# Optimization experiments

Measured on AMD Instinct MI355X. Metric: run time of the kernel, lower is better.

## Reference

```python
import jax, jax.numpy as jnp
import numpy as np

N, E, IN_CH, HIDDEN, N_CLASS, LAYERS = 2048, 1024, 512, 512, 40, 10
EPS = 1e-10


def setup_inputs() -> dict:
    key = jax.random.key(0)
    ks = jax.random.split(key, 6)
    x = jax.random.normal(ks[0], (1, N, IN_CH), jnp.float32)
    H = (jax.random.uniform(ks[1], (N, E)) < 0.02).astype(jnp.float32)
    # symmetric Laplacian-like operator so eigh is meaningful
    M = jax.random.normal(ks[2], (1, N, N), jnp.float32) / np.sqrt(N).astype(np.float32)
    L = 0.5 * (M + jnp.swapaxes(M, 1, 2))
    W_first = jax.random.normal(ks[3], (HIDDEN, IN_CH), jnp.float32) * 0.05
    W_mid = jax.random.normal(ks[4], (LAYERS - 2, HIDDEN, HIDDEN), jnp.float32) * 0.05
    W_last = jax.random.normal(ks[5], (N_CLASS, HIDDEN), jnp.float32) * 0.05
    return {"x": x, "L": L, "H": H, "W_first": W_first, "W_mid": W_mid, "W_last": W_last}


def _expanded_energy(x2d, H, d_v, d_e):
    # Vectorized form of the nested hyperedge/pair loop:
    # sum_e sum_{u<v in e} H_ue*H_ve/(d_e+eps) * ||x_u/sqrt(dv_u+eps) - x_v/sqrt(dv_v+eps)||^2
    # = sum_e (s_e * q_e - ||m_e||^2) / (d_e + eps)  with binary H (w_e = 1)
    y = x2d / jnp.sqrt(d_v + EPS)[:, None]          # [N, F]
    q = H.T @ jnp.sum(y * y, axis=1)                # [E] sum_u H_ue ||y_u||^2
    m = H.T @ y                                     # [E, F]
    s = jnp.sum(H, axis=0)                          # [E] edge degrees (= d_e)
    return jnp.sum((s * q - jnp.sum(m * m, axis=1)) / (d_e + EPS))


def reference(x, L, H, W_first, W_mid, W_last):
    weights = [W_first] + [W_mid[i] for i in range(LAYERS - 2)] + [W_last]
    d_v = jnp.sum(H, axis=1)
    d_e = jnp.sum(H, axis=0)
    # eigh of L is identical every layer in the original; compute once
    eigvals = jnp.linalg.eigh(L)[0]                 # [B, N]
    spectral_gap = jnp.min(jnp.where(eigvals > 1e-10, eigvals, jnp.inf))
    energies, energies_exp, snorms = [], [], []
    for i, W in enumerate(weights):
        x = jax.nn.relu(jnp.einsum('bnm,bmf->bnf', L, x) @ W.T)
        xs, Ls = x[0], L[0]                         # @torch.no_grad() blocks
        energies.append(jnp.trace(xs.T @ (Ls @ xs)))
        energies_exp.append(_expanded_energy(xs, H, d_v, d_e))
        snorms.append(jnp.linalg.norm(W, ord=2))
        # dropout skipped (eval-mode reference)
    log_probs = jax.nn.log_softmax(x, axis=1)       # dim=1 as in original
    return (log_probs, jnp.stack(energies), jnp.stack(energies_exp),
            jnp.stack(snorms), spectral_gap)
```

## Files before the change

### kernel.cpp

```cpp
#include <hip/hip_runtime.h>
#include <math.h>


typedef __attribute__((ext_vector_type(8))) short short8;
typedef __attribute__((ext_vector_type(4))) float f32x4;

#define NSHIFT 256

__device__ inline ushort bf16_rne(float f) {
    unsigned int u = __float_as_uint(f);
    return (ushort)((u + 0x7FFFu + ((u >> 16) & 1u)) >> 16);
}
__device__ inline float bf16_tof(ushort h) {
    return __uint_as_float(((unsigned int)h) << 16);
}

__device__ __forceinline__ void pbar(int* bar, int e, int w, int nwg) {
    __syncthreads();
    if (threadIdx.x == 0) {
        __threadfence();
        __hip_atomic_store(bar + 16 + w*16, e, __ATOMIC_RELAXED, __HIP_MEMORY_SCOPE_AGENT);
    }
    if (w == 0) {
        if ((int)threadIdx.x < nwg) {
            while (__hip_atomic_load(bar + 16 + threadIdx.x*16, __ATOMIC_RELAXED,
                                     __HIP_MEMORY_SCOPE_AGENT) < e)
                __builtin_amdgcn_s_sleep(1);
        }
        __syncthreads();
        if (threadIdx.x == 0)
            __hip_atomic_store(bar, e, __ATOMIC_RELEASE, __HIP_MEMORY_SCOPE_AGENT);
    } else {
        if (threadIdx.x == 0) {
            while (__hip_atomic_load(bar, __ATOMIC_RELAXED, __HIP_MEMORY_SCOPE_AGENT) < e)
                __builtin_amdgcn_s_sleep(8);
        }
    }
    if (threadIdx.x == 0) __threadfence();
    __syncthreads();
}

__global__ void init_misc(int* bar) {
    for (int j = blockIdx.x*256 + threadIdx.x; j < 16384; j += gridDim.x*256) bar[j] = 0;
}

template<bool TA, bool TB>
__device__ __forceinline__
void tile64g(const float* __restrict__ A, int lda,
             const float* __restrict__ B, int ldb,
             int bm, int bn, int k0, int k1, float acc[4][4],
             float (*sA)[68], float (*sB)[68])
{
    const int tid = threadIdx.x;
    const int tx = tid & 15, ty = tid >> 4;
    for (int kk = k0; kk < k1; kk += 16) {
        __syncthreads();
        for (int i = tid; i < 1024; i += 256) {
            int m, k2;
            if (TA) { m = i & 63; k2 = i >> 6; } else { k2 = i & 15; m = i >> 4; }
            sA[k2][m] = TA ? A[(size_t)(kk + k2)*lda + bm + m]
                           : A[(size_t)(bm + m)*lda + kk + k2];
        }
        for (int i = tid; i < 1024; i += 256) {
            int n, k2;
            if (TB) { k2 = i & 15; n = i >> 4; } else { n = i & 63; k2 = i >> 6; }
            sB[k2][n] = TB ? B[(size_t)(bn + n)*ldb + kk + k2]
                           : B[(size_t)(kk + k2)*ldb + bn + n];
        }
        __syncthreads();
        #pragma unroll
        for (int k2 = 0; k2 < 16; ++k2) {
            float4 a4 = *(const float4*)&sA[k2][ty*4];
            float4 b4 = *(const float4*)&sB[k2][tx*4];
            float av[4] = {a4.x, a4.y, a4.z, a4.w};
            float bv[4] = {b4.x, b4.y, b4.z, b4.w};
            #pragma unroll
            for (int i2 = 0; i2 < 4; ++i2)
                #pragma unroll
                for (int j2 = 0; j2 < 4; ++j2)
                    acc[i2][j2] += av[i2] * bv[j2];
        }
    }
}

template<bool TA, bool TB>
__device__ __forceinline__
void tile64d(const float* __restrict__ A, int lda,
             const float* __restrict__ B, int ldb,
             int bm, int bn, int k0, int k1, float acc[4][4],
             float (*sA)[16][68], float (*sB)[16][68])
{
    const int tid = threadIdx.x;
    const int tx = tid & 15, ty = tid >> 4;
    float ra[4], rb[4];
    auto ldregs = [&](int kk) {
        #pragma unroll
        for (int q = 0; q < 4; ++q) {
            int i = tid + q*256;
            if (TA) { int m = i & 63, k2 = i >> 6; ra[q] = A[(size_t)(kk + k2)*lda + bm + m]; }
            else    { int k2 = i & 15, m = i >> 4; ra[q] = A[(size_t)(bm + m)*lda + kk + k2]; }
            if (TB) { int k3 = i & 15, n = i >> 4; rb[q] = B[(size_t)(bn + n)*ldb + kk + k3]; }
            else    { int k3 = i >> 6, n = i & 63; rb[q] = B[(size_t)(kk + k3)*ldb + bn + n]; }
        }
    };
    auto stlds = [&](int buf) {
        #pragma unroll
        for (int q = 0; q < 4; ++q) {
            int i = tid + q*256;
            if (TA) { int m = i & 63, k2 = i >> 6; sA[buf][k2][m] = ra[q]; }
            else    { int k2 = i & 15, m = i >> 4; sA[buf][k2][m] = ra[q]; }
            if (TB) { int k3 = i & 15, n = i >> 4; sB[buf][k3][n] = rb[q]; }
            else    { int k3 = i >> 6, n = i & 63; sB[buf][k3][n] = rb[q]; }
        }
    };
    const int nit = (k1 - k0) >> 4;
    ldregs(k0);
    stlds(0);
    for (int it = 0; it < nit; ++it) {
        const int buf = it & 1;
        if (it + 1 < nit) ldregs(k0 + (it + 1)*16);
        __syncthreads();
        #pragma unroll
        for (int k2 = 0; k2 < 16; ++k2) {
            float4 a4 = *(const float4*)&sA[buf][k2][ty*4];
            float4 b4 = *(const float4*)&sB[buf][k2][tx*4];
            float av[4] = {a4.x, a4.y, a4.z, a4.w};
            float bv[4] = {b4.x, b4.y, b4.z, b4.w};
            #pragma unroll
            for (int i2 = 0; i2 < 4; ++i2)
                #pragma unroll
                for (int j2 = 0; j2 < 4; ++j2)
                    acc[i2][j2] += av[i2] * bv[j2];
        }
        if (it + 1 < nit) { __syncthreads(); stlds(buf ^ 1); }
    }
}

__device__ __forceinline__ void store_tile(float* C, int ldc, int bm, float acc[4][4]) {
    int tx = threadIdx.x & 15, ty = threadIdx.x >> 4;
    #pragma unroll
    for (int i = 0; i < 4; ++i)
        #pragma unroll
        for (int j = 0; j < 4; ++j)
            C[(size_t)(bm + ty*4 + i)*ldc + tx*4 + j] = acc[i][j];
}

__global__ void init_q0(float* Q) {
    int idx = blockIdx.x*256 + threadIdx.x;
    if (idx < 2048*64) {
        int n = idx >> 6, c = idx & 63;
        Q[(size_t)n*2048 + c] = (n == c) ? 1.f : 0.f;
    }
}

__global__ __launch_bounds__(256)
void lz_LQ(const float* __restrict__ Lm, const float* __restrict__ Qs, float* __restrict__ Cp)
{
    __shared__ float sA[2][16][68], sB[2][16][68];
    int z = blockIdx.x, mt = blockIdx.y;
    float acc[4][4] = {};
    tile64d<false,false>(Lm, 2048, Qs, 2048, mt*64, 0, z*256, z*256 + 256, acc, sA, sB);
    store_tile(Cp + (size_t)z*131072, 64, mt*64, acc);
}

__global__ void lz_sumZ(const float* __restrict__ Cp, float* __restrict__ Z)
{
    int idx = blockIdx.x*256 + threadIdx.x;
    float v = 0.f;
    #pragma unroll
    for (int z = 0; z < 8; ++z) v += Cp[(size_t)z*131072 + idx];
    Z[idx] = v;
}

__global__ __launch_bounds__(256)
void lz_QTZ(const float* __restrict__ Qall, const float* __restrict__ Z, float* __restrict__ Cp)
{
    __shared__ float sA[2][16][68], sB[2][16][68];
    int z = blockIdx.x, b = blockIdx.y;
    float acc[4][4] = {};
    tile64d<true,false>(Qall, 2048, Z, 64, b*64, 0, z*256, z*256 + 256, acc, sA, sB);
    store_tile(Cp + (size_t)z*131072, 64, b*64, acc);
}

__global__ void lz_sumC(const float* __restrict__ Cp, float* __restrict__ Creo,
                        float* __restrict__ Ab, int s)
{
    int idx = blockIdx.x*256 + threadIdx.x;
    float v = 0.f;
    #pragma unroll
    for (int z = 0; z < 8; ++z) v += Cp[(size_t)z*131072 + idx];
    Creo[idx] = v;
    if ((idx >> 6) >= 64*s) Ab[(size_t)s*4096 + (idx - s*4096)] = v;
}

__global__ __launch_bounds__(256)
void lz_QC(const float* __restrict__ Qall, const float* __restrict__ Creo,
           float* __restrict__ Cp, int s)
{
    __shared__ float sA[2][16][68], sB[2][16][68];
    int z = blockIdx.x, mt = blockIdx.y;
    float acc[4][4] = {};
    for (int j = z; j <= s; j += 8)
        tile64d<false,false>(Qall, 2048, Creo, 64, mt*64, 0, j*64, j*64 + 64, acc, sA, sB);
    store_tile(Cp + (size_t)z*131072, 64, mt*64, acc);
}

__global__ __launch_bounds__(256)
void lz_finZ(float* __restrict__ Z, const float* __restrict__ Cp, int nz,
             double* __restrict__ Gp)
{
    __shared__ float zb[64][65];
    int w = blockIdx.x, tid = threadIdx.x;
    for (int idx = tid; idx < 4096; idx += 256) {
        size_t o = (size_t)w*4096 + idx;
        float v = Z[o];
        for (int z = 0; z < nz; ++z) v -= Cp[(size_t)z*131072 + o];
        Z[o] = v;
        zb[idx >> 6][idx & 63] = v;
    }
    __syncthreads();
    int tx = tid & 15, ty = tid >> 4;
    double acc[4][4] = {};
    for (int r = 0; r < 64; ++r) {
        float av[4], bv[4];
        #pragma unroll
        for (int q = 0; q < 4; ++q) { av[q] = zb[r][ty*4 + q]; bv[q] = zb[r][tx*4 + q]; }
        #pragma unroll
        for (int i = 0; i < 4; ++i)
            #pragma unroll
            for (int j = 0; j < 4; ++j)
                acc[i][j] += (double)av[i] * (double)bv[j];
    }
    #pragma unroll
    for (int i = 0; i < 4; ++i)
        #pragma unroll
        for (int j = 0; j < 4; ++j)
            Gp[(size_t)w*4096 + (size_t)(ty*4 + i)*64 + tx*4 + j] = acc[i][j];
}

__global__ __launch_bounds__(256)
void lz_chol(const double* __restrict__ Gp, float* __restrict__ RinvF, float* __restrict__ BbS)
{
    __shared__ double G[64][65];
    __shared__ double Xs[64][65];
    __shared__ double lv[64];
    int tid = threadIdx.x;
    for (int idx = tid; idx < 4096; idx += 256) {
        double g = 0.0;
        for (int z = 0; z < 32; ++z) g += Gp[(size_t)z*4096 + idx];
        G[idx>>6][idx&63] = g;
    }
    __syncthreads();
    for (int k = 0; k < 64; ++k) {
        if (tid < 64) {
            double rkk = sqrt(fmax(G[k][k], 1e-40));
            lv[tid] = (tid == k) ? rkk : ((tid > k) ? G[k][tid]/rkk : 0.0);
        }
        __syncthreads();
        if (tid < 64 && tid >= k) G[k][tid] = lv[tid];
        for (int idx = tid; idx < 4096; idx += 256) {
            int i = idx>>6, j = idx&63;
            if (i > k && j >= i) G[i][j] -= lv[i]*lv[j];
        }
        __syncthreads();
    }
    for (int idx = tid; idx < 4096; idx += 256) {
        int i = idx>>6, j = idx&63;
        BbS[idx] = (j >= i) ? (float)G[i][j] : 0.f;
        Xs[i][j] = 0.0;
    }
    __syncthreads();
    if (tid < 64) {
        int j = tid;
        for (int i = j; i >= 0; --i) {
            double s2 = (i == j) ? 1.0 : 0.0;
            for (int k2 = i + 1; k2 <= j; ++k2) s2 -= G[i][k2]*Xs[k2][j];
            Xs[i][j] = s2 / G[i][i];
        }
    }
    __syncthreads();
    for (int idx = tid; idx < 4096; idx += 256)
        RinvF[idx] = (float)Xs[idx>>6][idx&63];
}

__global__ __launch_bounds__(256)
void lz_apply(const float* __restrict__ Z, const float* __restrict__ Rinv, float* __restrict__ Qn)
{
    __shared__ float sA[2][16][68], sB[2][16][68];
    int w = blockIdx.x;
    float acc[4][4] = {};
    tile64d<false,false>(Z, 64, Rinv, 64, w*64, 0, 0, 64, acc, sA, sB);
    store_tile(Qn, 2048, w*64, acc);
}

__global__ void assemble_band(const float* Ab, const float* Bb, float* band) {
    int idx = blockIdx.x*256 + threadIdx.x;
    if (idx >= 2048*65) return;
    int c = idx / 65, r = idx % 65;
    int row = c + r;
    float v = 0.f;
    if (row < 2048) {
        int j = c >> 6, q = c & 63, rr = q + r;
        if (rr <= 63) {
            const float* A = Ab + (size_t)j*4096;
            v = 0.5f*(A[rr*64 + q] + A[q*64 + rr]);
        } else if (j < 31) {
            int p = rr - 64;
            v = Bb[(size_t)j*4096 + p*64 + q];
        }
    }
    band[idx] = v;
}

__device__ __forceinline__
void pack_item(int idx, const float* __restrict__ src, const float* __restrict__ dv,
               ushort* __restrict__ Bh, ushort* __restrict__ Bl,
               ushort* __restrict__ Ch, ushort* __restrict__ Cl)
{
    int l = idx & 63, t = idx >> 6;
    int nb = t & 31, kc = t >> 5;
    int col = nb*16 + (l & 15);
    int k0 = kc*32 + ((l >> 4) << 3);
    ushort h8[8], l8[8], sh8[8], sl8[8];
    #pragma unroll
    for (int j = 0; j < 8; ++j) {
        int k = k0 + j;
        float v = src[(size_t)k*512 + col];
        ushort hb = bf16_rne(v);
        h8[j] = hb; l8[j] = bf16_rne(v - bf16_tof(hb));
        if (Ch) {
            float t2 = v * (1.0f / sqrtf(dv[k] + 1e-10f));
            ushort hb2 = bf16_rne(t2);
            sh8[j] = hb2; sl8[j] = bf16_rne(t2 - bf16_tof(hb2));
        }
    }
    uint4 hv, lv;
    hv.x = (unsigned)h8[0] | ((unsigned)h8[1] << 16);
    hv.y = (unsigned)h8[2] | ((unsigned)h8[3] << 16);
    hv.z = (unsigned)h8[4] | ((unsigned)h8[5] << 16);
    hv.w = (unsigned)h8[6] | ((unsigned)h8[7] << 16);
    lv.x = (unsigned)l8[0] | ((unsigned)l8[1] << 16);
    lv.y = (unsigned)l8[2] | ((unsigned)l8[3] << 16);
    lv.z = (unsigned)l8[4] | ((unsigned)l8[5] << 16);
    lv.w = (unsigned)l8[6] | ((unsigned)l8[7] << 16);
    *(uint4*)(Bh + (size_t)idx*8) = hv;
    *(uint4*)(Bl + (size_t)idx*8) = lv;
    if (Ch) {
        uint4 shv, slv;
        shv.x = (unsigned)sh8[0] | ((unsigned)sh8[1] << 16);
        shv.y = (unsigned)sh8[2] | ((unsigned)sh8[3] << 16);
        shv.z = (unsigned)sh8[4] | ((unsigned)sh8[5] << 16);
        shv.w = (unsigned)sh8[6] | ((unsigned)sh8[7] << 16);
        slv.x = (unsigned)sl8[0] | ((unsigned)sl8[1] << 16);
        slv.y = (unsigned)sl8[2] | ((unsigned)sl8[3] << 16);
        slv.z = (unsigned)sl8[4] | ((unsigned)sl8[5] << 16);
        slv.w = (unsigned)sl8[6] | ((unsigned)sl8[7] << 16);
        *(uint4*)(Ch + (size_t)idx*8) = shv;
        *(uint4*)(Cl + (size_t)idx*8) = slv;
    }
}

__global__ void pack_both(const float* __restrict__ src, const float* __restrict__ dv,
                          ushort* __restrict__ Bh, ushort* __restrict__ Bl,
                          ushort* __restrict__ Ch, ushort* __restrict__ Cl)
{
    int idx = blockIdx.x*256 + threadIdx.x;
    if (idx < 131072) pack_item(idx, src, dv, Bh, Bl, Ch, Cl);
}

__global__ void pack_A_L(const float* __restrict__ src, int Kld, int MB,
                         ushort* __restrict__ Ah, ushort* __restrict__ Al, int total)
{
    int idx = blockIdx.x*256 + threadIdx.x;
    if (idx >= total) return;
    int l = idx & 63, t = idx >> 6;
    int mb = t % MB, kc = t / MB;
    int m = mb*16 + (l & 15);
    int k0 = kc*32 + ((l >> 4) << 3);
    const float* p = src + (size_t)m*Kld + k0;
    float4 a = *(const float4*)p, b = *(const float4*)(p + 4);
    float vv[8] = {a.x,a.y,a.z,a.w,b.x,b.y,b.z,b.w};
    ushort h8[8], l8[8];
    #pragma unroll
    for (int j = 0; j < 8; ++j) {
        ushort hb = bf16_rne(vv[j]);
        h8[j] = hb; l8[j] = bf16_rne(vv[j] - bf16_tof(hb));
    }
    uint4 hv, lv;
    hv.x = (unsigned)h8[0] | ((unsigned)h8[1] << 16);
    hv.y = (unsigned)h8[2] | ((unsigned)h8[3] << 16);
    hv.z = (unsigned)h8[4] | ((unsigned)h8[5] << 16);
    hv.w = (unsigned)h8[6] | ((unsigned)h8[7] << 16);
    lv.x = (unsigned)l8[0] | ((unsigned)l8[1] << 16);
    lv.y = (unsigned)l8[2] | ((unsigned)l8[3] << 16);
    lv.z = (unsigned)l8[4] | ((unsigned)l8[5] << 16);
    lv.w = (unsigned)l8[6] | ((unsigned)l8[7] << 16);
    *(uint4*)(Ah + (size_t)idx*8) = hv;
    *(uint4*)(Al + (size_t)idx*8) = lv;
}

__global__ void pack_A_T(const float* __restrict__ src, int Mld, int MB,
                         ushort* __restrict__ Ah, int total)
{
    int idx = blockIdx.x*256 + threadIdx.x;
    if (idx >= total) return;
    int l = idx & 63, t = idx >> 6;
    int mb = t % MB, kc = t / MB;
    int m = mb*16 + (l & 15);
    int k0 = kc*32 + ((l >> 4) << 3);
    ushort h8[8];
    #pragma unroll
    for (int j = 0; j < 8; ++j)
        h8[j] = bf16_rne(src[(size_t)(k0 + j)*Mld + m]);
    uint4 hv;
    hv.x = (unsigned)h8[0] | ((unsigned)h8[1] << 16);
    hv.y = (unsigned)h8[2] | ((unsigned)h8[3] << 16);
    hv.z = (unsigned)h8[4] | ((unsigned)h8[5] << 16);
    hv.w = (unsigned)h8[6] | ((unsigned)h8[7] << 16);
    *(uint4*)(Ah + (size_t)idx*8) = hv;
}

__device__ __forceinline__
void mfma_task(int t, const ushort* __restrict__ Lph, const ushort* __restrict__ Lpl,
               const ushort* __restrict__ Bh, const ushort* __restrict__ Bl,
               const ushort* __restrict__ Htp,
               const ushort* __restrict__ Bqh, const ushort* __restrict__ Bql,
               float* __restrict__ U, float* __restrict__ ME,
               ushort (*lA)[4096], ushort (*lB)[4096])
{
    const bool isU = (t < 64);
    const ushort* Ah = isU ? Lph : Htp;
    const ushort* Al = isU ? Lpl : nullptr;
    const ushort* Xh = isU ? Bh : Bqh;
    const ushort* Xl = isU ? Bl : Bql;
    float* C = isU ? U : ME;
    const int MB = isU ? 128 : 64;
    const int tmb = (isU ? (t >> 2) : ((t - 64) >> 2)) * 8;
    const int tnb = (t & 3) * 8;
    const int KC = 64;
    const int tid = threadIdx.x;
    const int lane = tid & 63, wave = tid >> 6;
    const int wr = wave >> 1, wc = wave & 1;

    f32x4 acc[4][4];
    #pragma unroll
    for (int i = 0; i < 4; ++i)
        #pragma unroll
        for (int j = 0; j < 4; ++j) acc[i][j] = (f32x4){0.f,0.f,0.f,0.f};

    uint4 rAh[2], rAl[2], rBh[2], rBl[2];
    auto loadregs = [&](int kc) {
        const uint4* pa = (const uint4*)(Ah + ((size_t)kc*MB + tmb)*512);
        rAh[0] = pa[tid]; rAh[1] = pa[tid + 256];
        if (Al) {
            const uint4* pl = (const uint4*)(Al + ((size_t)kc*MB + tmb)*512);
            rAl[0] = pl[tid]; rAl[1] = pl[tid + 256];
        }
        const uint4* pb = (const uint4*)(Xh + ((size_t)kc*32 + tnb)*512);
        rBh[0] = pb[tid]; rBh[1] = pb[tid + 256];
        const uint4* pc = (const uint4*)(Xl + ((size_t)kc*32 + tnb)*512);
        rBl[0] = pc[tid]; rBl[1] = pc[tid + 256];
    };

    loadregs(0);
    for (int kc = 0; kc < KC; ++kc) {
        __syncthreads();
        *(uint4*)&lA[0][tid*8]       = rAh[0];
        *(uint4*)&lA[0][(tid+256)*8] = rAh[1];
        if (Al) {
            *(uint4*)&lA[1][tid*8]       = rAl[0];
            *(uint4*)&lA[1][(tid+256)*8] = rAl[1];
        }
        *(uint4*)&lB[0][tid*8]       = rBh[0];
        *(uint4*)&lB[0][(tid+256)*8] = rBh[1];
        *(uint4*)&lB[1][tid*8]       = rBl[0];
        *(uint4*)&lB[1][(tid+256)*8] = rBl[1];
        if (kc + 1 < KC) loadregs(kc + 1);
        __syncthreads();

        short8 a_h[4], a_l[4], b_h[4], b_l[4];
        #pragma unroll
        for (int i = 0; i < 4; ++i) {
            a_h[i] = *(const short8*)&lA[0][(((wr*4 + i)*64) + lane)*8];
            if (Al) a_l[i] = *(const short8*)&lA[1][(((wr*4 + i)*64) + lane)*8];
        }
        #pragma unroll
        for (int j = 0; j < 4; ++j) {
            b_h[j] = *(const short8*)&lB[0][(((wc*4 + j)*64) + lane)*8];
            b_l[j] = *(const short8*)&lB[1][(((wc*4 + j)*64) + lane)*8];
        }
        #pragma unroll
        for (int i = 0; i < 4; ++i)
            #pragma unroll
            for (int j = 0; j < 4; ++j) {
                acc[i][j] = __builtin_amdgcn_mfma_f32_16x16x32_bf16(a_h[i], b_h[j], acc[i][j], 0, 0, 0);
                acc[i][j] = __builtin_amdgcn_mfma_f32_16x16x32_bf16(a_h[i], b_l[j], acc[i][j], 0, 0, 0);
                if (Al)
                    acc[i][j] = __builtin_amdgcn_mfma_f32_16x16x32_bf16(a_l[i], b_h[j], acc[i][j], 0, 0, 0);
            }
    }
    const int r0 = tmb*16 + wr*64, c0 = tnb*16 + wc*64;
    #pragma unroll
    for (int i = 0; i < 4; ++i)
        #pragma unroll
        for (int j = 0; j < 4; ++j) {
            int row = r0 + i*16 + ((lane >> 4) << 2);
            int col = c0 + j*16 + (lane & 15);
            #pragma unroll
            for (int r = 0; r < 4; ++r)
                C[(size_t)(row + r)*512 + col] = acc[i][j][r];
        }
}

__global__ __launch_bounds__(256, 2)
void mgemm_dual(const ushort* __restrict__ Lph, const ushort* __restrict__ Lpl,
                const ushort* __restrict__ Bh, const ushort* __restrict__ Bl,
                const ushort* __restrict__ Htp,
                const ushort* __restrict__ Bqh, const ushort* __restrict__ Bql,
                float* __restrict__ U, float* __restrict__ ME)
{
    __shared__ ushort lA[2][4096];
    __shared__ ushort lB[2][4096];
    int t = blockIdx.y * 4 + blockIdx.x;
    mfma_task(t, Lph, Lpl, Bh, Bl, Htp, Bqh, Bql, U, ME, lA, lB);
}

__global__ __launch_bounds__(256, 1)
void mlp_persist(float* __restrict__ u, float* __restrict__ h,
                 const float* __restrict__ Wf, const float* __restrict__ Wm,
                 const ushort* __restrict__ Lph, const ushort* __restrict__ Lpl,
                 const ushort* __restrict__ Htp,
                 ushort* __restrict__ bpkh, ushort* __restrict__ bpkl,
                 ushort* __restrict__ bqh, ushort* __restrict__ bql,
                 const float* __restrict__ H, const float* __restrict__ dv,
                 const float* __restrict__ de,
                 float* __restrict__ mEb, float* __restrict__ srow,
                 float* __restrict__ qpart,
                 float* __restrict__ parts512, float* __restrict__ parts16,
                 float* __restrict__ outp, int* __restrict__ bar)
{
    const int w = blockIdx.x, tid = threadIdx.x;
    __shared__ char smem[35072];
    __shared__ float red4[4];
    float (*sA)[68] = (float(*)[68])smem;
    float (*sB)[68] = (float(*)[68])(smem + 4352);
    ushort (*lA)[4096] = (ushort(*)[4096])smem;
    ushort (*lB)[4096] = (ushort(*)[4096])(smem + 16384);
    int ep = 0;

    for (int k = 0; k < 9; ++k) {
        const float* W = (k == 0) ? Wf : Wm + (size_t)(k-1)*262144;
        if (w == 0 && k > 0 && tid < 64) {
            float s = parts512[tid] + parts512[tid+64] + parts512[tid+128] + parts512[tid+192];
            for (int o = 32; o; o >>= 1) s += __shfl_down(s, o, 64);
            float x = (tid < 16) ? parts16[tid] : 0.f;
            for (int o = 32; o; o >>= 1) x += __shfl_down(x, o, 64);
            if (tid == 0) { outp[81920 + k - 1] = s; outp[81930 + k - 1] = x; }
        }
        {
            int mt = w >> 3, nt = w & 7;
            float acc[4][4] = {};
            tile64g<false,true>(u, 512, W, 512, mt*64, nt*64, 0, 512, acc, sA, sB);
            int tx = tid & 15, ty = tid >> 4;
            #pragma unroll
            for (int i = 0; i < 4; ++i)
                #pragma unroll
                for (int j = 0; j < 4; ++j)
                    h[(size_t)(mt*64 + ty*4 + i)*512 + nt*64 + tx*4 + j] = fmaxf(acc[i][j], 0.f);
        }
        pbar(bar, ++ep, w, 256);
        for (int it = w*256 + tid; it < 131072; it += 65536)
            pack_item(it, h, dv, bpkh, bpkl, bqh, bql);
        {
            int lane = tid & 63;
            #pragma unroll
            for (int g = 0; g < 2; ++g) {
                int row = w*8 + g*4 + (tid >> 6);
                float rs = 1.0f / sqrtf(dv[row] + 1e-10f);
                float ss = 0.f;
                for (int f = lane; f < 512; f += 64) {
                    float t2 = h[(size_t)row*512 + f] * rs;
                    ss += t2*t2;
                }
                for (int o = 32; o; o >>= 1) ss += __shfl_down(ss, o, 64);
                if (lane == 0) srow[row] = ss;
            }
        }
        pbar(bar, ++ep, w, 256);
        if (w < 96) {
            mfma_task(w, Lph, Lpl, bpkh, bpkl, Htp, bqh, bql, u, mEb, lA, lB);
        } else if (w < 128) {
            int task = w - 96;
            int e = (task & 3)*256 + tid;
            int zc = task >> 2;
            float s = 0.f;
            for (int n = zc*256; n < zc*256 + 256; ++n) s += H[(size_t)n*1024 + e] * srow[n];
            qpart[(size_t)zc*1024 + e] = s;
        }
        pbar(bar, ++ep, w, 256);
        if (w < 16) {
            int wave = tid >> 6, lane = tid & 63;
            float acc = 0.f;
            for (int t2 = 0; t2 < 16; ++t2) {
                int e = w*64 + wave*16 + t2;
                float me2 = 0.f;
                for (int f = lane; f < 512; f += 64) { float v = mEb[(size_t)e*512 + f]; me2 += v*v; }
                for (int o = 32; o; o >>= 1) me2 += __shfl_down(me2, o, 64);
                if (lane == 0) {
                    float q = 0.f;
                    for (int z = 0; z < 8; ++z) q += qpart[(size_t)z*1024 + e];
                    acc += (de[e]*q - me2) / (de[e] + 1e-10f);
                }
            }
            if (lane == 0) red4[wave] = acc;
            __syncthreads();
            if (tid == 0) parts16[w] = red4[0]+red4[1]+red4[2]+red4[3];
            __syncthreads();
        }
        {
            int lane = tid & 63;
            float dd = 0.f;
            #pragma unroll
            for (int g = 0; g < 2; ++g) {
                int row = w*8 + g*4 + (tid >> 6);
                for (int f = lane; f < 512; f += 64)
                    dd += h[(size_t)row*512 + f] * u[(size_t)row*512 + f];
            }
            for (int o = 32; o; o >>= 1) dd += __shfl_down(dd, o, 64);
            __syncthreads();
            if (lane == 0) red4[tid >> 6] = dd;
            __syncthreads();
            if (tid == 0) parts512[w] = red4[0]+red4[1]+red4[2]+red4[3];
        }
        pbar(bar, ++ep, w, 256);
    }
    if (w == 0 && tid < 64) {
        float s = parts512[tid] + parts512[tid+64] + parts512[tid+128] + parts512[tid+192];
        for (int o = 32; o; o >>= 1) s += __shfl_down(s, o, 64);
        float x = (tid < 16) ? parts16[tid] : 0.f;
        for (int o = 32; o; o >>= 1) x += __shfl_down(x, o, 64);
        if (tid == 0) { outp[81928] = s; outp[81938] = x; }
    }
}

template<bool TA, bool TB>
__global__ __launch_bounds__(256)
void gemm_f32(const float* A, int lda, const float* B, int ldb,
              float* C, int ldc, float* Cpart,
              int M, int N, int K, float alpha, float beta, int relu)
{
    const int S = (int)gridDim.z, z = (int)blockIdx.z;
    const int kchunk = (K + S - 1) / S;
    const int k0 = z * kchunk;
    const int k1 = (K < k0 + kchunk) ? K : (k0 + kchunk);
    const int bm = blockIdx.y * 64, bn = blockIdx.x * 64;
    __shared__ float As[16][68];
    __shared__ float Bs[16][68];
    const int tid = threadIdx.x;
    const int tx = tid & 15, ty = tid >> 4;
    float acc[4][4] = {};
    for (int kk = k0; kk < k1; kk += 16) {
        for (int i = tid; i < 1024; i += 256) {
            int m, k;
            if (TA) { m = i & 63; k = i >> 6; } else { k = i & 15; m = i >> 4; }
            int gm = bm + m, gk = kk + k;
            float v = 0.f;
            if (gm < M && gk < k1) v = TA ? A[(size_t)gk*lda + gm] : A[(size_t)gm*lda + gk];
            As[k][m] = v;
        }
        for (int i = tid; i < 1024; i += 256) {
            int n, k;
            if (TB) { k = i & 15; n = i >> 4; } else { n = i & 63; k = i >> 6; }
            int gn = bn + n, gk = kk + k;
            float v = 0.f;
            if (gn < N && gk < k1) v = TB ? B[(size_t)gn*ldb + gk] : B[(size_t)gk*ldb + gn];
            Bs[k][n] = v;
        }
        __syncthreads();
        #pragma unroll
        for (int k = 0; k < 16; ++k) {
            float4 ra4 = *reinterpret_cast<const float4*>(&As[k][ty*4]);
            float4 rb4 = *reinterpret_cast<const float4*>(&Bs[k][tx*4]);
            float ra[4] = {ra4.x, ra4.y, ra4.z, ra4.w};
            float rb[4] = {rb4.x, rb4.y, rb4.z, rb4.w};
            #pragma unroll
            for (int i = 0; i < 4; ++i)
                #pragma unroll
                for (int j = 0; j < 4; ++j)
                    acc[i][j] += ra[i] * rb[j];
        }
        __syncthreads();
    }
    if (S == 1) {
        #pragma unroll
        for (int i = 0; i < 4; ++i) {
            int gm = bm + ty*4 + i;
            if (gm >= M) continue;
            #pragma unroll
            for (int j = 0; j < 4; ++j) {
                int gn = bn + tx*4 + j;
                if (gn >= N) continue;
                float v = alpha * acc[i][j];
                if (beta != 0.f) v += beta * C[(size_t)gm*ldc + gn];
                if (relu) v = fmaxf(v, 0.f);
                C[(size_t)gm*ldc + gn] = v;
            }
        }
    } else {
        float* P = Cpart + (size_t)z * M * N;
        #pragma unroll
        for (int i = 0; i < 4; ++i) {
            int gm = bm + ty*4 + i;
            if (gm >= M) continue;
            #pragma unroll
            for (int j = 0; j < 4; ++j) {
                int gn = bn + tx*4 + j;
                if (gn >= N) continue;
                P[(size_t)gm*N + gn] = alpha * acc[i][j];
            }
        }
    }
}

__global__ void reduce_parts(const float* Cpart, float* C, int M, int N, int ldc,
                             int S, float beta, int relu)
{
    int total = M * N;
    for (int idx = blockIdx.x*256 + threadIdx.x; idx < total; idx += gridDim.x*256) {
        float s = 0.f;
        for (int z = 0; z < S; ++z) s += Cpart[(size_t)z*total + idx];
        int mm = idx / N, nn = idx % N;
        float v = s;
        if (beta != 0.f) v += beta * C[(size_t)mm*ldc + nn];
        if (relu) v = fmaxf(v, 0.f);
        C[(size_t)mm*ldc + nn] = v;
    }
}

__global__ void row_deg(const float* H, float* dv) {
    int row = blockIdx.x*4 + (threadIdx.x >> 6);
    int lane = threadIdx.x & 63;
    if (row >= 2048) return;
    float s = 0.f;
    for (int e = lane; e < 1024; e += 64) s += H[(size_t)row*1024 + e];
    for (int o = 32; o; o >>= 1) s += __shfl_down(s, o, 64);
    if (lane == 0) dv[row] = s;
}

__global__ void coldot_part(const float* H, const float* w, float* part) {
    int e = blockIdx.x*256 + threadIdx.x;
    int zc = blockIdx.y;
    float s = 0.f;
    if (w) {
        for (int n = zc*256; n < zc*256 + 256; ++n) s += H[(size_t)n*1024 + e] * w[n];
    } else {
        for (int n = zc*256; n < zc*256 + 256; ++n) s += H[(size_t)n*1024 + e];
    }
    part[(size_t)zc*1024 + e] = s;
}
__global__ void coldot_fin(const float* part, float* outp) {
    int e = blockIdx.x*256 + threadIdx.x;
    float s = 0.f;
    for (int z = 0; z < 8; ++z) s += part[(size_t)z*1024 + e];
    outp[e] = s;
}

__global__ void dotsrow(const float* h, const float* u, int F, const float* dv,
                        float* srow, float* yout, float* parts)
{
    int row = blockIdx.x*4 + (threadIdx.x >> 6);
    int lane = threadIdx.x & 63;
    __shared__ float a4[4];
    float rs = 1.0f / sqrtf(dv[row] + 1e-10f);
    float ss = 0.f, dd = 0.f;
    for (int f = lane; f < F; f += 64) {
        float hv = h[(size_t)row*F + f];
        float t = hv * rs;
        if (yout) yout[(size_t)row*F + f] = t;
        ss += t*t;
        dd += hv * u[(size_t)row*F + f];
    }
    for (int o = 32; o; o >>= 1) { ss += __shfl_down(ss, o, 64); dd += __shfl_down(dd, o, 64); }
    if (lane == 0) { srow[row] = ss; a4[threadIdx.x >> 6] = dd; }
    __syncthreads();
    if (threadIdx.x == 0) parts[blockIdx.x] = a4[0]+a4[1]+a4[2]+a4[3];
}

__global__ void edge_energy(const float* m, int F, const float* de, const float* qpart,
                            float* partials) {
    int wave = threadIdx.x >> 6, lane = threadIdx.x & 63;
    __shared__ float acc4[4];
    float acc = 0.f;
    for (int t = 0; t < 16; ++t) {
        int e = blockIdx.x*64 + wave*16 + t;
        float me2 = 0.f;
        for (int f = lane; f < F; f += 64) { float v = m[(size_t)e*F + f]; me2 += v*v; }
        for (int o = 32; o; o >>= 1) me2 += __shfl_down(me2, o, 64);
        if (lane == 0) {
            float q = 0.f;
            for (int z = 0; z < 8; ++z) q += qpart[(size_t)z*1024 + e];
            acc += (de[e]*q - me2) / (de[e] + 1e-10f);
        }
    }
    if (lane == 0) acc4[wave] = acc;
    __syncthreads();
    if (threadIdx.x == 0) partials[blockIdx.x] = acc4[0]+acc4[1]+acc4[2]+acc4[3];
}

__global__ void finalize2(const float* p512, const float* p16, float* oe, float* ox) {
    __shared__ float red[256];
    int tid = threadIdx.x;
    red[tid] = p512[tid] + p512[tid + 256];
    __syncthreads();
    for (int st = 128; st; st >>= 1) { if (tid < st) red[tid] += red[tid+st]; __syncthreads(); }
    if (tid == 0) *oe = red[0];
    __syncthreads();
    red[tid] = (tid < 16) ? p16[tid] : 0.f;
    __syncthreads();
    for (int st = 128; st; st >>= 1) { if (tid < st) red[tid] += red[tid+st]; __syncthreads(); }
    if (tid == 0) *ox = red[0];
}

__global__ void logsoftmax(const float* xf, float* outp) {
    __shared__ float red[256];
    int c = blockIdx.x, tid = threadIdx.x;
    float mx = -3.0e38f;
    for (int n = tid; n < 2048; n += 256) mx = fmaxf(mx, xf[(size_t)n*40 + c]);
    red[tid] = mx; __syncthreads();
    for (int st = 128; st; st >>= 1) { if (tid < st) red[tid] = fmaxf(red[tid], red[tid+st]); __syncthreads(); }
    mx = red[0]; __syncthreads();
    float s = 0.f;
    for (int n = tid; n < 2048; n += 256) s += expf(xf[(size_t)n*40 + c] - mx);
    red[tid] = s; __syncthreads();
    for (int st = 128; st; st >>= 1) { if (tid < st) red[tid] += red[tid+st]; __syncthreads(); }
    float lse = mx + logf(red[0]);
    for (int n = tid; n < 2048; n += 256) outp[(size_t)n*40 + c] = xf[(size_t)n*40 + c] - lse;
}

__global__ __launch_bounds__(256)
void band_count(const float* __restrict__ band, const double* __restrict__ shifts,
                int* __restrict__ counts)
{
    __shared__ double win[66][66];
    const int tid = threadIdx.x;
    const double sigma = shifts[blockIdx.x];
    int ei[9], ej[9];
    {
        int i = 1, S = 0;
        #pragma unroll
        for (int k = 0; k < 9; ++k) {
            int T = tid + k*256;
            if (T < 2080) {
                while (S + (65 - i) <= T) { S += 65 - i; ++i; }
                ei[k] = i; ej[k] = i + (T - S);
            } else { ei[k] = 0; ej[k] = 0; }
        }
    }
    for (int idx = tid; idx < 65*65; idx += 256) {
        int c0 = idx / 65, r = idx % 65;
        win[c0][r] = (double)band[c0*65 + r] - (r == 0 ? sigma : 0.0);
    }
    __syncthreads();
    int cnt = 0;
    for (int c = 0; c < 2048; ++c) {
        const int p = c % 66;
        double d = win[p][0];
        if (fabs(d) < 1e-100) d = (d < 0 ? -1e-100 : 1e-100);
        if (d < 0) cnt++;
        double inv = 1.0 / d;
        #pragma unroll
        for (int k = 0; k < 9; ++k) {
            int i = ei[k];
            if (i) {
                int j = ej[k];
                int r2 = p + i; if (r2 >= 66) r2 -= 66;
                win[r2][j - i] -= win[p][i] * inv * win[p][j];
            }
        }
        int cn = c + 65;
        int slot = p + 65; if (slot >= 66) slot -= 66;
        if (tid < 65)
            win[slot][tid] = (cn < 2048)
                ? ((double)band[(size_t)cn*65 + tid] - (tid == 0 ? sigma : 0.0)) : 0.0;
        __syncthreads();
    }
    if (tid == 0) counts[blockIdx.x] = cnt;
}

__global__ void bisect(double* shifts, const int* counts, double* st, float* gap_out, int mode) {
    if (threadIdx.x != 0) return;
    if (mode == 0) {
        shifts[0] = 1e-10;
        double l0 = log(1e-6), l1 = log(0.5);
        for (int i = 1; i < NSHIFT; ++i) shifts[i] = exp(l0 + (l1 - l0)*(i - 1)/(double)(NSHIFT - 2));
        return;
    }
    if (mode == 1) {
        int n0 = counts[0];
        double lo = shifts[NSHIFT-1], hi = 1.5;
        for (int i = 1; i < NSHIFT; ++i) if (counts[i] > n0) { lo = shifts[i-1]; hi = shifts[i]; break; }
        st[0] = lo; st[1] = hi; st[2] = (double)n0;
        for (int i = 0; i < NSHIFT; ++i) shifts[i] = lo + (hi - lo)*(i + 1)/(double)(NSHIFT + 1);
        return;
    }
    int n0 = (int)st[2];
    double lo = st[0], hi = st[1];
    double nlo = shifts[NSHIFT-1], nhi = hi;
    for (int i = 0; i < NSHIFT; ++i) if (counts[i] > n0) { nhi = shifts[i]; nlo = (i == 0) ? lo : shifts[i-1]; break; }
    *gap_out = (float)(0.5*(nlo + nhi));
}

__global__ __launch_bounds__(256)
void gram9(const float* __restrict__ Wf, const float* __restrict__ Wm, float* __restrict__ sG)
{
    int mi = blockIdx.z;
    const float* W = (mi == 0) ? Wf : Wm + (size_t)(mi-1)*262144;
    __shared__ float sA[16][68], sB[16][68];
    int tid = threadIdx.x, tx = tid & 15, ty = tid >> 4;
    int bm = blockIdx.y*64, bn = blockIdx.x*64;
    float acc[4][4] = {};
    for (int kk = 0; kk < 512; kk += 16) {
        __syncthreads();
        for (int i = tid; i < 1024; i += 256) { int m = i&63, k = i>>6; sA[k][m] = W[(size_t)(kk+k)*512 + bm+m]; }
        for (int i = tid; i < 1024; i += 256) { int n = i&63, k = i>>6; sB[k][n] = W[(size_t)(kk+k)*512 + bn+n]; }
        __syncthreads();
        #pragma unroll
        for (int k = 0; k < 16; ++k) {
            float4 a4 = *(const float4*)&sA[k][ty*4];
            float4 b4 = *(const float4*)&sB[k][tx*4];
            float av[4]={a4.x,a4.y,a4.z,a4.w}, bv[4]={b4.x,b4.y,b4.z,b4.w};
            #pragma unroll
            for (int i = 0; i < 4; ++i)
                #pragma unroll
                for (int j = 0; j < 4; ++j) acc[i][j] += av[i]*bv[j];
        }
    }
    float* C = sG + (size_t)mi*262144;
    #pragma unroll
    for (int i = 0; i < 4; ++i)
        #pragma unroll
        for (int j = 0; j < 4; ++j)
            C[(size_t)(bm + ty*4 + i)*512 + bn + tx*4 + j] = acc[i][j];
}

__global__ __launch_bounds__(256)
void snorm_lanczos(const float* Gall, const float* Wl, float* outp) {
    int w = blockIdx.x, tid = threadIdx.x;
    int n = (w < 9) ? 512 : 40;
    const float* G = Gall + (size_t)w*262144;
    __shared__ float g40[1600];
    __shared__ float v[512], vp[512], wv[512], red[256];
    __shared__ float al[32], be[32];
    if (w == 9) {
        for (int p = tid; p < 1600; p += 256) {
            int i = p / 40, j = p % 40;
            float s = 0.f;
            for (int k2 = 0; k2 < 512; ++k2) s += Wl[(size_t)i*512 + k2]*Wl[(size_t)j*512 + k2];
            g40[p] = s;
        }
        __syncthreads();
    }
    float inv0 = 1.f / sqrtf((float)n);
    for (int i = tid; i < n; i += 256) { v[i] = inv0; vp[i] = 0.f; }
    __syncthreads();
    float beta_prev = 0.f;
    for (int s = 0; s < 32; ++s) {
        for (int r = tid; r < n; r += 256) {
            float sum = 0.f;
            if (w < 9) { const float* row = G + (size_t)r*512; for (int k2 = 0; k2 < 512; ++k2) sum += row[k2]*v[k2]; }
            else       { const float* row = &g40[r*40];        for (int k2 = 0; k2 < 40;  ++k2) sum += row[k2]*v[k2]; }
            wv[r] = sum;
        }
        __syncthreads();
        float p = 0.f;
        for (int i = tid; i < n; i += 256) p += v[i]*wv[i];
        red[tid] = p; __syncthreads();
        for (int st = 128; st; st >>= 1) { if (tid < st) red[tid] += red[tid+st]; __syncthreads(); }
        float alpha = red[0]; __syncthreads();
        for (int i = tid; i < n; i += 256) wv[i] -= alpha*v[i] + beta_prev*vp[i];
        __syncthreads();
        p = 0.f;
        for (int i = tid; i < n; i += 256) p += wv[i]*wv[i];
        red[tid] = p; __syncthreads();
        for (int st = 128; st; st >>= 1) { if (tid < st) red[tid] += red[tid+st]; __syncthreads(); }
        float beta = sqrtf(fmaxf(red[0], 0.f)); __syncthreads();
        if (tid == 0) { al[s] = alpha; be[s] = beta; }
        float ib = 1.f / fmaxf(beta, 1e-20f);
        for (int i = tid; i < n; i += 256) { float t = v[i]; vp[i] = t; v[i] = wv[i]*ib; }
        beta_prev = beta;
        __syncthreads();
    }
    if (tid == 0) {
        float hi = 0.f;
        for (int s = 0; s < 32; ++s) {
            float g2 = al[s] + be[s] + (s ? be[s-1] : 0.f);
            hi = fmaxf(hi, g2);
        }
        float lo = 0.f;
        for (int it = 0; it < 48; ++it) {
            float mid = 0.5f*(lo + hi);
            float d = al[0] - mid; int c2 = (d < 0.f);
            for (int s = 1; s < 32; ++s) {
                float dp = d;
                if (fabsf(dp) < 1e-25f) dp = (dp < 0.f) ? -1e-25f : 1e-25f;
                d = (al[s] - mid) - be[s-1]*be[s-1]/dp;
                c2 += (d < 0.f);
            }
            if (c2 == 32) hi = mid; else lo = mid;
        }
        outp[w] = sqrtf(fmaxf(0.5f*(lo + hi), 0.f));
    }
}

static void gemm64(hipStream_t st, int ta, int tb, int M, int N, int K,
                   const float* A, int lda, const float* B, int ldb,
                   float* C, int ldc, float alpha, float beta, int relu,
                   float* Cpart, int S)
{
    dim3 grid((unsigned)((N + 63)/64), (unsigned)((M + 63)/64), (unsigned)S);
    if (!ta && !tb)      gemm_f32<false,false><<<grid,256,0,st>>>(A,lda,B,ldb,C,ldc,Cpart,M,N,K,alpha,beta,relu);
    else if (!ta && tb)  gemm_f32<false,true ><<<grid,256,0,st>>>(A,lda,B,ldb,C,ldc,Cpart,M,N,K,alpha,beta,relu);
    else if (ta && !tb)  gemm_f32<true ,false><<<grid,256,0,st>>>(A,lda,B,ldb,C,ldc,Cpart,M,N,K,alpha,beta,relu);
    else                 gemm_f32<true ,true ><<<grid,256,0,st>>>(A,lda,B,ldb,C,ldc,Cpart,M,N,K,alpha,beta,relu);
    if (S > 1) {
        int total = M * N;
        int g = (total + 255)/256; if (g > 2048) g = 2048;
        reduce_parts<<<g,256,0,st>>>(Cpart, C, M, N, ldc, S, beta, relu);
    }
}

extern "C" void kernel_launch(void* const* d_in, const int* in_sizes, int n_in,
                              void* d_out, int out_size, void* d_ws, size_t ws_size,
                              hipStream_t stream)
{
    (void)in_sizes; (void)n_in; (void)out_size; (void)ws_size;
    const float* X  = (const float*)d_in[0];
    const float* Lm = (const float*)d_in[1];
    const float* H  = (const float*)d_in[2];
    const float* Wf = (const float*)d_in[3];
    const float* Wm = (const float*)d_in[4];
    const float* Wl = (const float*)d_in[5];
    float* out = (float*)d_out;

    float* ws = (float*)d_ws;
    size_t off = 0;
    auto alloc = [&](size_t n) { float* p = ws + off; off += (n + 255) & ~(size_t)255; return p; };
    float* Lph_f  = alloc((size_t)2097152);
    float* Lpl_f  = alloc((size_t)2097152);
    float* Htp_f  = alloc((size_t)1048576);
    float* bpkh_f = alloc((size_t)524288);
    float* bpkl_f = alloc((size_t)524288);
    float* h      = alloc((size_t)2048*512);
    float* u      = alloc((size_t)2048*512);
    float* mEb    = alloc((size_t)1024*512);
    float* Cpart  = alloc((size_t)1024*1024);
    float* dv     = alloc(2048);
    float* de     = alloc(1024);
    float* srow   = alloc(2048);
    float* qpart  = alloc(8*1024);
    float* parts512 = alloc(512);
    float* parts16  = alloc(256);
    double* shifts  = (double*)alloc(2*NSHIFT);
    double* bstate  = (double*)alloc(8);
    int* counts     = (int*)alloc(NSHIFT);
    int* barbase    = (int*)alloc(16384);

    ushort* Lph  = (ushort*)Lph_f;
    ushort* Lpl  = (ushort*)Lpl_f;
    ushort* Htp  = (ushort*)Htp_f;
    ushort* bpkh = (ushort*)bpkh_f;
    ushort* bpkl = (ushort*)bpkl_f;
    ushort* bqh  = (ushort*)Cpart;
    ushort* bql  = (ushort*)(Cpart + 524288);
    int* barM = barbase;
    float* Qall  = Lph_f;
    float* Z     = Htp_f;
    float* Creo  = Htp_f + 131072;
    float* Ab    = Htp_f + 262144;
    float* Bb    = Htp_f + 393216;
    float* band  = Htp_f + 524288;
    float* Rinv  = Htp_f + 658432;
    double* GpD  = (double*)bpkh_f;
    float* sG    = Qall;
    float* h9  = mEb;
    float* y9  = mEb + 131072;
    float* mE9 = mEb + 262144;

    init_misc<<<16,256,0,stream>>>(barbase);
    pack_A_L<<<2048,256,0,stream>>>(Lm, 2048, 128, Lph, Lpl, 524288);
    pack_A_T<<<1024,256,0,stream>>>(H, 1024, 64, Htp, 262144);
    row_deg<<<512,256,0,stream>>>(H, dv);
    coldot_part<<<dim3(4,8),256,0,stream>>>(H, nullptr, qpart);
    coldot_fin<<<4,256,0,stream>>>(qpart, de);

    pack_both<<<512,256,0,stream>>>(X, dv, bpkh, bpkl, nullptr, nullptr);
    mgemm_dual<<<dim3(4,16),256,0,stream>>>(Lph, Lpl, bpkh, bpkl, Htp, bqh, bql, u, mEb);

    mlp_persist<<<256,256,0,stream>>>(u, h, Wf, Wm, Lph, Lpl, Htp,
                                      bpkh, bpkl, bqh, bql, H, dv, de,
                                      mEb, srow, qpart, parts512, parts16, out, barM);

    gemm64(stream, 0,1, 2048,40,512, u,512, Wl,512, h9,40, 1.f,0.f,1, Cpart,8);
    gemm64(stream, 0,0, 2048,40,2048, Lm,2048, h9,40, u,40, 1.f,0.f,0, Cpart,8);
    dotsrow<<<512,256,0,stream>>>(h9, u, 40, dv, srow, y9, parts512);
    coldot_part<<<dim3(4,8),256,0,stream>>>(H, srow, qpart);
    gemm64(stream, 1,0, 1024,40,2048, H,1024, y9,40, mE9,40, 1.f,0.f,0, Cpart,8);
    edge_energy<<<16,256,0,stream>>>(mE9, 40, de, qpart, parts16);
    finalize2<<<1,256,0,stream>>>(parts512, parts16, out + 81929, out + 81939);
    logsoftmax<<<40,256,0,stream>>>(h9, out);

    init_q0<<<512,256,0,stream>>>(Qall);
    for (int s = 0; s < 32; ++s) {
        lz_LQ<<<dim3(8,32),256,0,stream>>>(Lm, Qall + 64*s, Cpart);
        lz_sumZ<<<512,256,0,stream>>>(Cpart, Z);
        lz_QTZ<<<dim3(8,(unsigned)(s+1)),256,0,stream>>>(Qall, Z, Cpart);
        lz_sumC<<<(s+1)*16,256,0,stream>>>(Cpart, Creo, Ab, s);
        if (s == 31) break;
        int nz = (s + 1 < 8) ? s + 1 : 8;
        lz_QC<<<dim3((unsigned)nz,32),256,0,stream>>>(Qall, Creo, Cpart, s);
        lz_finZ<<<32,256,0,stream>>>(Z, Cpart, nz, GpD);
        lz_chol<<<1,256,0,stream>>>(GpD, Rinv, Bb + (size_t)s*4096);
        lz_apply<<<32,256,0,stream>>>(Z, Rinv, Qall + (size_t)64*(s+1));
    }
    assemble_band<<<520,256,0,stream>>>(Ab, Bb, band);

    bisect<<<1,64,0,stream>>>(shifts, counts, bstate, out + 81950, 0);
    band_count<<<NSHIFT,256,0,stream>>>(band, shifts, counts);
    bisect<<<1,64,0,stream>>>(shifts, counts, bstate, out + 81950, 1);
    band_count<<<NSHIFT,256,0,stream>>>(band, shifts, counts);
    bisect<<<1,64,0,stream>>>(shifts, counts, bstate, out + 81950, 3);

    gram9<<<dim3(8,8,9),256,0,stream>>>(Wf, Wm, sG);
    snorm_lanczos<<<10,256,0,stream>>>(sG, Wl, out + 81940);
}
```

Baseline: 15.50 ms.

## Fuse bf16 packing and row-norm partials into GEMM epilogue, dropping a grid barrier

The persistent MLP kernel now stages each 64x64 output tile of the ReLU GEMM in shared memory and packs the split-bf16 operands (plain and degree-scaled) directly from it. It also computes per-tile partial row sums of squares, written as 8 partials per row. This removes one grid-wide barrier per layer and the global re-read of h for packing and row norms. The q-computation stage now sums the 8 partials per row, which adds redundant reads in that stage.

```diff
diff --git a/kernel.cpp b/kernel.cpp
--- a/kernel.cpp
+++ b/kernel.cpp
@@ -534,7 +534,7 @@
                  ushort* __restrict__ bqh, ushort* __restrict__ bql,
                  const float* __restrict__ H, const float* __restrict__ dv,
                  const float* __restrict__ de,
-                 float* __restrict__ mEb, float* __restrict__ srow,
+                 float* __restrict__ mEb, float* __restrict__ srowp,
                  float* __restrict__ qpart,
                  float* __restrict__ parts512, float* __restrict__ parts16,
                  float* __restrict__ outp, int* __restrict__ bar)
@@ -542,11 +542,15 @@
     const int w = blockIdx.x, tid = threadIdx.x;
     __shared__ char smem[35072];
     __shared__ float red4[4];
+    __shared__ float sRs[64];
     float (*sA)[68] = (float(*)[68])smem;
     float (*sB)[68] = (float(*)[68])(smem + 4352);
+    float (*sT)[65] = (float(*)[65])smem;
     ushort (*lA)[4096] = (ushort(*)[4096])smem;
     ushort (*lB)[4096] = (ushort(*)[4096])(smem + 16384);
     int ep = 0;
+    const int mt = w >> 3, nt = w & 7;
+    const int tx = tid & 15, ty = tid >> 4;
 
     for (int k = 0; k < 9; ++k) {
         const float* W = (k == 0) ? Wf : Wm + (size_t)(k-1)*262144;
@@ -558,32 +562,64 @@
             if (tid == 0) { outp[81920 + k - 1] = s; outp[81930 + k - 1] = x; }
         }
         {
-            int mt = w >> 3, nt = w & 7;
             float acc[4][4] = {};
             tile64g<false,true>(u, 512, W, 512, mt*64, nt*64, 0, 512, acc, sA, sB);
-            int tx = tid & 15, ty = tid >> 4;
+            __syncthreads();
+            if (tid < 64) sRs[tid] = 1.0f / sqrtf(dv[mt*64 + tid] + 1e-10f);
             #pragma unroll
             for (int i = 0; i < 4; ++i)
                 #pragma unroll
-                for (int j = 0; j < 4; ++j)
-                    h[(size_t)(mt*64 + ty*4 + i)*512 + nt*64 + tx*4 + j] = fmaxf(acc[i][j], 0.f);
-        }
-        pbar(bar, ++ep, w, 256);
-        for (int it = w*256 + tid; it < 131072; it += 65536)
-            pack_item(it, h, dv, bpkh, bpkl, bqh, bql);
-        {
-            int lane = tid & 63;
+                for (int j = 0; j < 4; ++j) {
+                    float v = fmaxf(acc[i][j], 0.f);
+                    h[(size_t)(mt*64 + ty*4 + i)*512 + nt*64 + tx*4 + j] = v;
+                    sT[ty*4 + i][tx*4 + j] = v;
+                }
+            __syncthreads();
             #pragma unroll
-            for (int g = 0; g < 2; ++g) {
-                int row = w*8 + g*4 + (tid >> 6);
-                float rs = 1.0f / sqrtf(dv[row] + 1e-10f);
+            for (int q = 0; q < 2; ++q) {
+                int it = tid + q*256;
+                int a = it >> 8, rem = it & 255;
+                int b = rem >> 6, lane = rem & 63;
+                int cl = b*16 + (lane & 15);
+                int r0 = a*32 + ((lane >> 4) << 3);
+                int idxg = (((2*mt + a)*32 + (4*nt + b))*64 + lane);
+                ushort h8[8], l8[8], sh8[8], sl8[8];
+                #pragma unroll
+                for (int j = 0; j < 8; ++j) {
+                    float v = sT[r0 + j][cl];
+                    ushort hb = bf16_rne(v);
+                    h8[j] = hb; l8[j] = bf16_rne(v - bf16_tof(hb));
+                    float t2 = v * sRs[r0 + j];
+                    ushort hb2 = bf16_rne(t2);
+                    sh8[j] = hb2; sl8[j] = bf16_rne(t2 - bf16_tof(hb2));
+                }
+                uint4 hv, lv, shv, slv;
+                hv.x = (unsigned)h8[0] | ((unsigned)h8[1] << 16);
+                hv.y = (unsigned)h8[2] | ((unsigned)h8[3] << 16);
+                hv.z = (unsigned)h8[4] | ((unsigned)h8[5] << 16);
+                hv.w = (unsigned)h8[6] | ((unsigned)h8[7] << 16);
+                lv.x = (unsigned)l8[0] | ((unsigned)l8[1] << 16);
+                lv.y = (unsigned)l8[2] | ((unsigned)l8[3] << 16);
+                lv.z = (unsigned)l8[4] | ((unsigned)l8[5] << 16);
+                lv.w = (unsigned)l8[6] | ((unsigned)l8[7] << 16);
+                shv.x = (unsigned)sh8[0] | ((unsigned)sh8[1] << 16);
+                shv.y = (unsigned)sh8[2] | ((unsigned)sh8[3] << 16);
+                shv.z = (unsigned)sh8[4] | ((unsigned)sh8[5] << 16);
+                shv.w = (unsigned)sh8[6] | ((unsigned)sh8[7] << 16);
+                slv.x = (unsigned)sl8[0] | ((unsigned)sl8[1] << 16);
+                slv.y = (unsigned)sl8[2] | ((unsigned)sl8[3] << 16);
+                slv.z = (unsigned)sl8[4] | ((unsigned)sl8[5] << 16);
+                slv.w = (unsigned)sl8[6] | ((unsigned)sl8[7] << 16);
+                *(uint4*)(bpkh + (size_t)idxg*8) = hv;
+                *(uint4*)(bpkl + (size_t)idxg*8) = lv;
+                *(uint4*)(bqh  + (size_t)idxg*8) = shv;
+                *(uint4*)(bql  + (size_t)idxg*8) = slv;
+            }
+            if (tid < 64) {
+                float rs = sRs[tid];
                 float ss = 0.f;
-                for (int f = lane; f < 512; f += 64) {
-                    float t2 = h[(size_t)row*512 + f] * rs;
-                    ss += t2*t2;
-                }
-                for (int o = 32; o; o >>= 1) ss += __shfl_down(ss, o, 64);
-                if (lane == 0) srow[row] = ss;
+                for (int c = 0; c < 64; ++c) { float v = sT[tid][c]; ss += v*v; }
+                srowp[(size_t)nt*2048 + mt*64 + tid] = ss * rs * rs;
             }
         }
         pbar(bar, ++ep, w, 256);
@@ -594,7 +630,12 @@
             int e = (task & 3)*256 + tid;
             int zc = task >> 2;
             float s = 0.f;
-            for (int n = zc*256; n < zc*256 + 256; ++n) s += H[(size_t)n*1024 + e] * srow[n];
+            for (int n = zc*256; n < zc*256 + 256; ++n) {
+                float sr = 0.f;
+                #pragma unroll
+                for (int p2 = 0; p2 < 8; ++p2) sr += srowp[(size_t)p2*2048 + n];
+                s += H[(size_t)n*1024 + e] * sr;
+            }
             qpart[(size_t)zc*1024 + e] = s;
         }
         pbar(bar, ++ep, w, 256);
@@ -1054,6 +1095,7 @@
     float* u      = alloc((size_t)2048*512);
     float* mEb    = alloc((size_t)1024*512);
     float* Cpart  = alloc((size_t)1024*1024);
+    float* srowp  = alloc((size_t)8*2048);
     float* dv     = alloc(2048);
     float* de     = alloc(1024);
     float* srow   = alloc(2048);
@@ -1098,7 +1140,7 @@
 
     mlp_persist<<<256,256,0,stream>>>(u, h, Wf, Wm, Lph, Lpl, Htp,
                                       bpkh, bpkl, bqh, bql, H, dv, de,
-                                      mEb, srow, qpart, parts512, parts16, out, barM);
+                                      mEb, srowp, qpart, parts512, parts16, out, barM);
 
     gemm64(stream, 0,1, 2048,40,512, u,512, Wl,512, h9,40, 1.f,0.f,1, Cpart,8);
     gemm64(stream, 0,0, 2048,40,2048, Lm,2048, h9,40, u,40, 1.f,0.f,0, Cpart,8);
```

New measurement: 15.37 ms, median of 2. About the same (-0.8%).
